# Performance work log

Measured on AMD Instinct MI355X. Metric: run time of the kernel, lower is better.

The kernel has to match this reference:

```python
import jax, jax.numpy as jnp
import numpy as np

B, L, D, H, S = 2, 2048, 1024, 16, 4
Dh = D // H
EPS = 1e-5


def setup_inputs() -> dict:
    key = jax.random.key(0)
    ks = jax.random.split(key, 12)
    sc = 0.02
    w = lambda k, shape: (jax.random.normal(k, shape, jnp.float32) * sc)
    M = 2 * S  # number of MHA blocks / dense linears
    inp = {
        "response": jax.random.normal(ks[0], (B, L, D), jnp.float32),
        "mask": jnp.broadcast_to(jnp.tril(jnp.ones((L, L), bool)), (B, L, L)),
        "Wq": w(ks[1], (M, D, D)), "bq": w(ks[2], (M, D)),
        "Wk": w(ks[3], (M, D, D)), "bk": w(ks[4], (M, D)),
        "Wv": w(ks[5], (M, D, D)), "bv": w(ks[6], (M, D)),
        "Wo": w(ks[7], (M, D, D)), "bo": w(ks[8], (M, D)),
        "Wd": w(ks[9], (M, D, D)), "bd": w(ks[10], (M, D)),
    }
    return inp


def _ln(x):
    # fresh LayerNorm(d) with default weight=1, bias=0, eps=1e-5
    m = jnp.mean(x, axis=-1, keepdims=True)
    v = jnp.mean((x - m) ** 2, axis=-1, keepdims=True)
    return (x - m) * jax.lax.rsqrt(v + EPS)


def _linear(x, W, b):
    # torch Linear: x @ W.T + b
    return jnp.einsum('bld,od->blo', x, W) + b


def _mha(x, i, mask, Wq, bq, Wk, bk, Wv, bv, Wo, bo):
    # self-attention: q = k = v = x
    split = lambda y: y.reshape(B, L, H, Dh).transpose(0, 2, 1, 3)  # (B,H,L,Dh)
    q = split(_linear(x, Wq[i], bq[i]))
    k = split(_linear(x, Wk[i], bk[i]))
    v = split(_linear(x, Wv[i], bv[i]))
    scores = jnp.einsum('bhqd,bhkd->bhqk', q, k) / jnp.sqrt(jnp.float32(Dh))
    if mask is not None:
        scores = jnp.where(mask[:, None, :, :], scores, -jnp.inf)
    p = jnp.nan_to_num(jax.nn.softmax(scores, axis=-1))
    o = jnp.einsum('bhqk,bhkd->bhqd', p, v).transpose(0, 2, 1, 3).reshape(B, L, D)
    return _linear(o, Wo[i], bo[i])


def reference(response, mask, Wq, bq, Wk, bk, Wv, bv, Wo, bo, Wd, bd):
    x = response
    for i in range(S):
        # masked self-attention + residual + LN
        x = _ln(x + _mha(x, 2 * i, mask, Wq, bq, Wk, bk, Wv, bv, Wo, bo))
        # encoder-attention sublayer (encMem is None -> unmasked self-attention)
        x = _ln(x + _mha(x, 2 * i + 1, None, Wq, bq, Wk, bk, Wv, bv, Wo, bo))
        # dense: linear[2i](LeakyReLU(linear[2i+1](x)))
        h = jax.nn.leaky_relu(_linear(x, Wd[2 * i + 1], bd[2 * i + 1]), negative_slope=0.01)
        h = _linear(h, Wd[2 * i], bd[2 * i])
        x = _ln(x + h)
    return x
```

## Files before the change

kernel.cpp:

```cpp
#include <hip/hip_runtime.h>
#include <stdint.h>
#include <stddef.h>

typedef __attribute__((ext_vector_type(8))) _Float16 f16x8;
typedef __attribute__((ext_vector_type(4))) _Float16 f16x4;
typedef __attribute__((ext_vector_type(4))) float    f32x4;

#define NB 2
#define NL 2048
#define ND 1024
#define NH 16
#define NROWS (NB*NL)

__device__ __forceinline__ void async16(void* lds, const void* g) {
  __builtin_amdgcn_global_load_lds(
      (const __attribute__((address_space(1))) void*)g,
      (__attribute__((address_space(3))) void*)lds, 16, 0, 0);
}

struct CvtArgs { const float* in[5]; _Float16* out[5]; };

__global__ __launch_bounds__(256) void cvt_all(CvtArgs a, int n16)
{
  const float* in  = a.in[blockIdx.z];
  _Float16*   out  = a.out[blockIdx.z];
  for (int i = blockIdx.x * blockDim.x + threadIdx.x; i < n16;
       i += gridDim.x * blockDim.x) {
    const f32x4* src = (const f32x4*)in + 4 * (size_t)i;
    f32x4 v0 = __builtin_nontemporal_load(src);
    f32x4 v1 = __builtin_nontemporal_load(src + 1);
    f32x4 v2 = __builtin_nontemporal_load(src + 2);
    f32x4 v3 = __builtin_nontemporal_load(src + 3);
    f16x8 o0 = {(_Float16)v0[0], (_Float16)v0[1], (_Float16)v0[2], (_Float16)v0[3],
                (_Float16)v1[0], (_Float16)v1[1], (_Float16)v1[2], (_Float16)v1[3]};
    f16x8 o1 = {(_Float16)v2[0], (_Float16)v2[1], (_Float16)v2[2], (_Float16)v2[3],
                (_Float16)v3[0], (_Float16)v3[1], (_Float16)v3[2], (_Float16)v3[3]};
    ((f16x8*)out)[2 * (size_t)i]     = o0;
    ((f16x8*)out)[2 * (size_t)i + 1] = o1;
  }
}

__global__ __launch_bounds__(256) void init_x(
    const float* __restrict__ r, _Float16* __restrict__ xh, int n8)
{
  for (int i = blockIdx.x * blockDim.x + threadIdx.x; i < n8;
       i += gridDim.x * blockDim.x) {
    float4 v0 = ((const float4*)r)[2 * i];
    float4 v1 = ((const float4*)r)[2 * i + 1];
    f16x8 o = {(_Float16)v0.x, (_Float16)v0.y, (_Float16)v0.z, (_Float16)v0.w,
               (_Float16)v1.x, (_Float16)v1.y, (_Float16)v1.z, (_Float16)v1.w};
    ((f16x8*)xh)[i] = o;
  }
}

struct GArgs {
  const _Float16* A;
  const _Float16* B[3];
  const float*    bias[3];
  void*           out[3];
  int             mode[3];
  int             ksplit;
};

__global__ __launch_bounds__(256, 2) void gemm_bt(GArgs ga)
{
  __shared__ _Float16 As[2][128 * 64];
  __shared__ _Float16 Bs[2][128 * 64];
  const int tid = threadIdx.x;
  const int w = tid >> 6, l = tid & 63;
  const int ql = l & 15, g = l >> 4;
  const int z = blockIdx.z;
  const int widx = ga.ksplit ? 0 : (blockIdx.x >> 3);
  const _Float16* Bw  = ga.B[widx];
  const float*   bias = ga.bias[widx];
  void*          outp = ga.ksplit ? ga.out[z] : ga.out[widx];
  const int      mode = ga.mode[widx];
  const int kbeg = ga.ksplit ? z * (ND / 2) : 0;
  const int kend = ga.ksplit ? kbeg + ND / 2 : ND;
  const bool dobias = (!ga.ksplit) || (z == 0);
  const int brow = blockIdx.y * 128;
  const int bcol = (blockIdx.x & 7) * 128;
  const int wm = w >> 1, wn = w & 1;
  f32x4 acc[4][4] = {};

  const int srow = w * 32 + (l >> 3);
  const int scol = ((l & 7) ^ (l >> 3)) << 3;
  const _Float16* Ag = ga.A + (size_t)(brow + srow) * ND + scol;
  const _Float16* Bg = Bw   + (size_t)(bcol + srow) * ND + scol;

#define STAGE(buf, k0_)                                                  \
  {                                                                      \
    _Float16* AsW = &As[buf][w * 2048];                                  \
    _Float16* BsW = &Bs[buf][w * 2048];                                  \
    _Pragma("unroll")                                                    \
    for (int i = 0; i < 4; ++i) {                                        \
      async16(AsW + i * 512, Ag + (size_t)i * 8 * ND + (k0_));           \
      async16(BsW + i * 512, Bg + (size_t)i * 8 * ND + (k0_));           \
    }                                                                    \
  }

  STAGE(0, kbeg);
  for (int k0 = kbeg; k0 < kend; k0 += 64) {
    const int cur = ((k0 - kbeg) >> 6) & 1;
    if (k0 + 64 < kend) {
      STAGE(cur ^ 1, k0 + 64);
      asm volatile("s_waitcnt vmcnt(8)" ::: "memory");
    } else {
      asm volatile("s_waitcnt vmcnt(0)" ::: "memory");
    }
    __builtin_amdgcn_s_barrier();
    __builtin_amdgcn_s_setprio(1);
#pragma unroll
    for (int ks = 0; ks < 64; ks += 32) {
      const int cx = (ks + g * 8) ^ ((ql & 7) << 3);
      f16x8 af[4], bf[4];
#pragma unroll
      for (int mi = 0; mi < 4; ++mi)
        af[mi] = *(const f16x8*)&As[cur][(wm * 64 + mi * 16 + ql) * 64 + cx];
#pragma unroll
      for (int nj = 0; nj < 4; ++nj)
        bf[nj] = *(const f16x8*)&Bs[cur][(wn * 64 + nj * 16 + ql) * 64 + cx];
#pragma unroll
      for (int mi = 0; mi < 4; ++mi)
#pragma unroll
        for (int nj = 0; nj < 4; ++nj)
          acc[mi][nj] = __builtin_amdgcn_mfma_f32_16x16x32_f16(
              af[mi], bf[nj], acc[mi][nj], 0, 0, 0);
    }
    __builtin_amdgcn_s_setprio(0);
    asm volatile("s_waitcnt lgkmcnt(0)" ::: "memory");
    __builtin_amdgcn_s_barrier();
  }
#undef STAGE

  const int colb = bcol + wn * 64;
  const int rowb = brow + wm * 64 + g * 4;
  if (mode == 3) {
    _Float16* vt = (_Float16*)outp;
    const int bb = rowb >> 11;
#pragma unroll
    for (int nj = 0; nj < 4; ++nj) {
      const int col = colb + nj * 16 + ql;
      const float bv = bias[col];
      const int hh = col >> 6, d = col & 63;
      _Float16* vrow = vt + ((size_t)((bb * NH + hh) * 64 + d)) * NL;
#pragma unroll
      for (int mi = 0; mi < 4; ++mi) {
        const int krow = (rowb + mi * 16) & (NL - 1);
        f16x4 o;
#pragma unroll
        for (int r = 0; r < 4; ++r) o[r] = (_Float16)(acc[mi][nj][r] + bv);
        *(f16x4*)(vrow + krow) = o;
      }
    }
  } else {
    _Float16* oh = (_Float16*)outp;
#pragma unroll
    for (int nj = 0; nj < 4; ++nj) {
      const int col = colb + nj * 16 + ql;
      const float bv = dobias ? bias[col] : 0.f;
#pragma unroll
      for (int mi = 0; mi < 4; ++mi) {
#pragma unroll
        for (int r = 0; r < 4; ++r) {
          float v = acc[mi][nj][r] + bv;
          if (mode == 2) v = v > 0.f ? v : 0.01f * v;
          oh[(size_t)(rowb + mi * 16 + r) * ND + col] = (_Float16)v;
        }
      }
    }
  }
}

template<bool CAUSAL>
__global__ __launch_bounds__(512, 4) void attn_fwd(
    const _Float16* __restrict__ Q, const _Float16* __restrict__ K,
    const _Float16* __restrict__ Vt, _Float16* __restrict__ O)
{
  __shared__ _Float16 kv[3][2][64 * 64];
  __shared__ unsigned int pls[8][8 * 34];
  const int tid = threadIdx.x;
  const int w = tid >> 6, l = tid & 63;
  const int ql = l & 15, g = l >> 4;
  const int bi = blockIdx.x;
  const int within = bi >> 3;
  const int p = (bi & 7) + 8 * (within >> 4);
  const int h = p & 15, b = p >> 4;
  const int qt_raw = within & 15;
  const int qt = (CAUSAL && b) ? (NL / 128 - 1 - qt_raw) : qt_raw;
  const int qrow = qt * 128 + w * 16 + ql;

  const _Float16* Qp = Q + (size_t)(b * NL + qrow) * ND + h * 64 + g * 8;
  const f16x8 bq0 = *(const f16x8*)Qp;
  const f16x8 bq1 = *(const f16x8*)(Qp + 32);

  const int srow = w * 8 + (l >> 3);
  const int scol = ((l & 7) ^ (l >> 3)) << 3;
  const _Float16* Kg = K  + ((size_t)(b * NL) + srow) * ND + h * 64 + scol;
  const _Float16* Vg = Vt + ((size_t)((b * NH + h) * 64 + srow)) * NL + scol;

  const int msk  = (ql & 7) << 3;
  const int offA = ql * 64 + ((     g * 8) ^ msk);
  const int offB = ql * 64 + ((32 + g * 8) ^ msk);

  unsigned int* pw = &pls[w][0];
  f32x4 ot[4] = {};
  f32x4 sum_acc = {};
  const f16x8 ones = {(_Float16)1.f, (_Float16)1.f, (_Float16)1.f, (_Float16)1.f,
                      (_Float16)1.f, (_Float16)1.f, (_Float16)1.f, (_Float16)1.f};
  const int ntiles = CAUSAL ? (qt * 2 + 2) : (NL / 64);
  const float SCL = 0.125f * 1.44269504089f;
  const float M2  = 4.0f * 1.44269504089f;

  async16(&kv[0][0][w * 512], Kg);
  async16(&kv[0][1][w * 512], Vg);

  int cbuf = 0, sbuf = 1;
  for (int kt = 0; kt < ntiles; ++kt) {
    const size_t nk0 = (size_t)((kt + 1 < ntiles) ? kt + 1 : kt) * 64;
    async16(&kv[sbuf][0][w * 512], Kg + nk0 * ND);
    async16(&kv[sbuf][1][w * 512], Vg + nk0);
    asm volatile("s_waitcnt vmcnt(2)" ::: "memory");
    __builtin_amdgcn_s_barrier();

    const _Float16* kb = &kv[cbuf][0][0];
    const _Float16* vb = &kv[cbuf][1][0];
    const int k0 = kt * 64;
    f32x4 st[4] = {};
    __builtin_amdgcn_s_setprio(1);
#pragma unroll
    for (int sub = 0; sub < 4; ++sub) {
      const f16x8 a0 = *(const f16x8*)&kb[sub * 1024 + offA];
      const f16x8 a1 = *(const f16x8*)&kb[sub * 1024 + offB];
      st[sub] = __builtin_amdgcn_mfma_f32_16x16x32_f16(a0, bq0, st[sub], 0, 0, 0);
      st[sub] = __builtin_amdgcn_mfma_f32_16x16x32_f16(a1, bq1, st[sub], 0, 0, 0);
    }
    __builtin_amdgcn_s_setprio(0);
    float pv[16];
#pragma unroll
    for (int sub = 0; sub < 4; ++sub)
#pragma unroll
      for (int r = 0; r < 4; ++r) {
        float p2 = exp2f(__builtin_fmaf(st[sub][r], SCL, -M2));
        if (CAUSAL && (k0 + sub * 16 + g * 4 + r) > qrow) p2 = 0.f;
        pv[sub * 4 + r] = p2;
      }

#pragma unroll
    for (int sub = 0; sub < 2; ++sub) {
      uint2 uu;
      uu.x = __builtin_bit_cast(unsigned int,
                __builtin_amdgcn_cvt_pkrtz(pv[sub * 4 + 0], pv[sub * 4 + 1]));
      uu.y = __builtin_bit_cast(unsigned int,
                __builtin_amdgcn_cvt_pkrtz(pv[sub * 4 + 2], pv[sub * 4 + 3]));
      *(uint2*)&pw[(sub * 4 + g) * 34 + 2 * ql] = uu;
    }
    {
      uint2 lo = *(const uint2*)&pw[(2 * g    ) * 34 + 2 * ql];
      uint2 hi = *(const uint2*)&pw[(2 * g + 1) * 34 + 2 * ql];
      uint4 ui; ui.x = lo.x; ui.y = lo.y; ui.z = hi.x; ui.w = hi.y;
      const f16x8 pf = __builtin_bit_cast(f16x8, ui);
      __builtin_amdgcn_s_setprio(1);
#pragma unroll
      for (int dt = 0; dt < 4; ++dt) {
        const f16x8 vf = *(const f16x8*)&vb[dt * 1024 + offA];
        ot[dt] = __builtin_amdgcn_mfma_f32_16x16x32_f16(vf, pf, ot[dt], 0, 0, 0);
      }
      sum_acc = __builtin_amdgcn_mfma_f32_16x16x32_f16(ones, pf, sum_acc, 0, 0, 0);
      __builtin_amdgcn_s_setprio(0);
    }
#pragma unroll
    for (int sub = 2; sub < 4; ++sub) {
      uint2 uu;
      uu.x = __builtin_bit_cast(unsigned int,
                __builtin_amdgcn_cvt_pkrtz(pv[sub * 4 + 0], pv[sub * 4 + 1]));
      uu.y = __builtin_bit_cast(unsigned int,
                __builtin_amdgcn_cvt_pkrtz(pv[sub * 4 + 2], pv[sub * 4 + 3]));
      *(uint2*)&pw[((sub - 2) * 4 + g) * 34 + 2 * ql] = uu;
    }
    {
      uint2 lo = *(const uint2*)&pw[(2 * g    ) * 34 + 2 * ql];
      uint2 hi = *(const uint2*)&pw[(2 * g + 1) * 34 + 2 * ql];
      uint4 ui; ui.x = lo.x; ui.y = lo.y; ui.z = hi.x; ui.w = hi.y;
      const f16x8 pf = __builtin_bit_cast(f16x8, ui);
      __builtin_amdgcn_s_setprio(1);
#pragma unroll
      for (int dt = 0; dt < 4; ++dt) {
        const f16x8 vf = *(const f16x8*)&vb[dt * 1024 + offB];
        ot[dt] = __builtin_amdgcn_mfma_f32_16x16x32_f16(vf, pf, ot[dt], 0, 0, 0);
      }
      sum_acc = __builtin_amdgcn_mfma_f32_16x16x32_f16(ones, pf, sum_acc, 0, 0, 0);
      __builtin_amdgcn_s_setprio(0);
    }
    cbuf = sbuf;
    sbuf = sbuf + 1 == 3 ? 0 : sbuf + 1;
  }

  const float inv = 1.f / sum_acc[0];
#pragma unroll
  for (int dt = 0; dt < 4; ++dt) {
    f16x4 o;
#pragma unroll
    for (int r = 0; r < 4; ++r) o[r] = (_Float16)(ot[dt][r] * inv);
    *(f16x4*)(O + (size_t)(b * NL + qrow) * ND + h * 64 + dt * 16 + g * 4) = o;
  }
}

template<bool FINAL>
__global__ __launch_bounds__(256) void resid_ln(
    const _Float16* __restrict__ xh_in, const _Float16* __restrict__ d0,
    const _Float16* __restrict__ d1,
    _Float16* __restrict__ xh_out, float* __restrict__ xf)
{
  const int row = blockIdx.x, tid = threadIdx.x;
  const f16x4 xv = ((const f16x4*)(xh_in + (size_t)row * ND))[tid];
  const f16x4 v0 = ((const f16x4*)(d0 + (size_t)row * ND))[tid];
  const f16x4 v1 = ((const f16x4*)(d1 + (size_t)row * ND))[tid];
  const float a = (float)xv[0] + (float)v0[0] + (float)v1[0];
  const float b = (float)xv[1] + (float)v0[1] + (float)v1[1];
  const float c = (float)xv[2] + (float)v0[2] + (float)v1[2];
  const float d = (float)xv[3] + (float)v0[3] + (float)v1[3];
  float s = a + b + c + d;
  float ss = a * a + b * b + c * c + d * d;
#pragma unroll
  for (int m = 1; m < 64; m <<= 1) {
    s  += __shfl_xor(s, m);
    ss += __shfl_xor(ss, m);
  }
  __shared__ float red[8];
  if ((tid & 63) == 0) { red[tid >> 6] = s; red[4 + (tid >> 6)] = ss; }
  __syncthreads();
  const float S  = red[0] + red[1] + red[2] + red[3];
  const float SS = red[4] + red[5] + red[6] + red[7];
  const float mean = S * (1.0f / ND);
  const float var  = SS * (1.0f / ND) - mean * mean;
  const float rstd = rsqrtf(fmaxf(var, 0.f) + 1e-5f);
  const float ya = (a - mean) * rstd, yb = (b - mean) * rstd;
  const float yc = (c - mean) * rstd, yd = (d - mean) * rstd;
  if (FINAL) {
    float4 y; y.x = ya; y.y = yb; y.z = yc; y.w = yd;
    ((float4*)(xf + (size_t)row * ND))[tid] = y;
  } else {
    f16x4 yh = {(_Float16)ya, (_Float16)yb, (_Float16)yc, (_Float16)yd};
    ((f16x4*)(xh_out + (size_t)row * ND))[tid] = yh;
  }
}

extern "C" void kernel_launch(void* const* d_in, const int* in_sizes, int n_in,
                              void* d_out, int out_size, void* d_ws, size_t ws_size,
                              hipStream_t stream)
{
  (void)in_sizes; (void)n_in; (void)out_size; (void)ws_size;
  const float* response = (const float*)d_in[0];
  const float* Wq = (const float*)d_in[2];
  const float* bq = (const float*)d_in[3];
  const float* Wk = (const float*)d_in[4];
  const float* bk = (const float*)d_in[5];
  const float* Wv = (const float*)d_in[6];
  const float* bv = (const float*)d_in[7];
  const float* Wo = (const float*)d_in[8];
  const float* bo = (const float*)d_in[9];
  const float* Wd = (const float*)d_in[10];
  const float* bd = (const float*)d_in[11];
  float* xf = (float*)d_out;

  const size_t MB = 1024 * 1024;
  char* p = (char*)d_ws;
  _Float16* Wq_h = (_Float16*)(p + 0 * MB);
  _Float16* Wk_h = (_Float16*)(p + 16 * MB);
  _Float16* Wv_h = (_Float16*)(p + 32 * MB);
  _Float16* Wo_h = (_Float16*)(p + 48 * MB);
  _Float16* Wd_h = (_Float16*)(p + 64 * MB);
  _Float16* xh   = (_Float16*)(p + 80 * MB);
  _Float16* Qh   = (_Float16*)(p + 88 * MB);
  _Float16* Kh   = (_Float16*)(p + 96 * MB);
  _Float16* Vth  = (_Float16*)(p + 104 * MB);
  _Float16* Oh   = (_Float16*)(p + 112 * MB);
  _Float16* h1   = Qh;
  _Float16* t0   = (_Float16*)(p + 96 * MB);
  _Float16* t1   = (_Float16*)(p + 104 * MB);

  const int wn16 = 8 * 1024 * 1024 / 16;
  CvtArgs ca = { { Wq, Wk, Wv, Wo, Wd }, { Wq_h, Wk_h, Wv_h, Wo_h, Wd_h } };
  cvt_all<<<dim3(1024, 1, 5), 256, 0, stream>>>(ca, wn16);
  init_x<<<1024, 256, 0, stream>>>(response, xh, NROWS * ND / 8);

  const dim3 g3(24, NROWS / 128, 1);
  const dim3 gs(8, NROWS / 128, 2);
  const dim3 gf(8, NROWS / 128, 1);
  const dim3 agrid(NL / 128 * NH * NB);

  for (int i = 0; i < 4; ++i) {
    for (int sub = 0; sub < 2; ++sub) {
      const int m = 2 * i + sub;
      const size_t wo = (size_t)m * MB;
      const size_t bf = (size_t)m * 1024;
      GArgs qkv = { xh,
                    { Wq_h + wo, Wk_h + wo, Wv_h + wo },
                    { bq + bf, bk + bf, bv + bf },
                    { Qh, Kh, Vth }, { 0, 0, 3 }, 0 };
      gemm_bt<<<g3, 256, 0, stream>>>(qkv);
      if (sub == 0) attn_fwd<true ><<<agrid, 512, 0, stream>>>(Qh, Kh, Vth, Oh);
      else          attn_fwd<false><<<agrid, 512, 0, stream>>>(Qh, Kh, Vth, Oh);
      GArgs oprj = { Oh,
                     { Wo_h + wo, nullptr, nullptr },
                     { bo + bf, nullptr, nullptr },
                     { t0, t1, nullptr }, { 0, 0, 0 }, 1 };
      gemm_bt<<<gs, 256, 0, stream>>>(oprj);
      resid_ln<false><<<NROWS, 256, 0, stream>>>(xh, t0, t1, xh, nullptr);
    }
    const size_t w1 = (size_t)(2 * i + 1) * MB, b1 = (size_t)(2 * i + 1) * 1024;
    const size_t w0 = (size_t)(2 * i) * MB,     b0 = (size_t)(2 * i) * 1024;
    GArgs f1 = { xh,
                 { Wd_h + w1, nullptr, nullptr },
                 { bd + b1, nullptr, nullptr },
                 { h1, nullptr, nullptr }, { 2, 0, 0 }, 0 };
    gemm_bt<<<gf, 256, 0, stream>>>(f1);
    GArgs f2 = { h1,
                 { Wd_h + w0, nullptr, nullptr },
                 { bd + b0, nullptr, nullptr },
                 { t0, t1, nullptr }, { 0, 0, 0 }, 1 };
    gemm_bt<<<gs, 256, 0, stream>>>(f2);
    if (i == 3) resid_ln<true ><<<NROWS, 256, 0, stream>>>(xh, t0, t1, nullptr, xf);
    else        resid_ln<false><<<NROWS, 256, 0, stream>>>(xh, t0, t1, xh, nullptr);
  }
}
```

Measured before the change: 1.184 ms.

## Single-buffer GEMM LDS tiles to raise occupancy to four blocks per CU

Replaces the double-buffered async global-to-LDS pipeline in the GEMM with a single-buffered load, wait, compute loop. LDS use is halved and launch bounds go from 2 to 4 blocks per CU. The aim is to hide memory latency through more resident blocks rather than intra-block prefetch. The trade is that each block now stalls on a full vmcnt(0) wait every K step, with no load/compute overlap inside the block.

```diff
diff --git a/kernel.cpp b/kernel.cpp
--- a/kernel.cpp
+++ b/kernel.cpp
@@ -62,10 +62,10 @@
   int             ksplit;
 };
 
-__global__ __launch_bounds__(256, 2) void gemm_bt(GArgs ga)
-{
-  __shared__ _Float16 As[2][128 * 64];
-  __shared__ _Float16 Bs[2][128 * 64];
+__global__ __launch_bounds__(256, 4) void gemm_bt(GArgs ga)
+{
+  __shared__ _Float16 As[128 * 64];
+  __shared__ _Float16 Bs[128 * 64];
   const int tid = threadIdx.x;
   const int w = tid >> 6, l = tid & 63;
   const int ql = l & 15, g = l >> 4;
@@ -88,26 +88,17 @@
   const _Float16* Ag = ga.A + (size_t)(brow + srow) * ND + scol;
   const _Float16* Bg = Bw   + (size_t)(bcol + srow) * ND + scol;
 
-#define STAGE(buf, k0_)                                                  \
-  {                                                                      \
-    _Float16* AsW = &As[buf][w * 2048];                                  \
-    _Float16* BsW = &Bs[buf][w * 2048];                                  \
-    _Pragma("unroll")                                                    \
-    for (int i = 0; i < 4; ++i) {                                        \
-      async16(AsW + i * 512, Ag + (size_t)i * 8 * ND + (k0_));           \
-      async16(BsW + i * 512, Bg + (size_t)i * 8 * ND + (k0_));           \
-    }                                                                    \
-  }
-
-  STAGE(0, kbeg);
   for (int k0 = kbeg; k0 < kend; k0 += 64) {
-    const int cur = ((k0 - kbeg) >> 6) & 1;
-    if (k0 + 64 < kend) {
-      STAGE(cur ^ 1, k0 + 64);
-      asm volatile("s_waitcnt vmcnt(8)" ::: "memory");
-    } else {
-      asm volatile("s_waitcnt vmcnt(0)" ::: "memory");
-    }
+    {
+      _Float16* AsW = &As[w * 2048];
+      _Float16* BsW = &Bs[w * 2048];
+#pragma unroll
+      for (int i = 0; i < 4; ++i) {
+        async16(AsW + i * 512, Ag + (size_t)i * 8 * ND + k0);
+        async16(BsW + i * 512, Bg + (size_t)i * 8 * ND + k0);
+      }
+    }
+    asm volatile("s_waitcnt vmcnt(0)" ::: "memory");
     __builtin_amdgcn_s_barrier();
     __builtin_amdgcn_s_setprio(1);
 #pragma unroll
@@ -116,10 +107,10 @@
       f16x8 af[4], bf[4];
 #pragma unroll
       for (int mi = 0; mi < 4; ++mi)
-        af[mi] = *(const f16x8*)&As[cur][(wm * 64 + mi * 16 + ql) * 64 + cx];
+        af[mi] = *(const f16x8*)&As[(wm * 64 + mi * 16 + ql) * 64 + cx];
 #pragma unroll
       for (int nj = 0; nj < 4; ++nj)
-        bf[nj] = *(const f16x8*)&Bs[cur][(wn * 64 + nj * 16 + ql) * 64 + cx];
+        bf[nj] = *(const f16x8*)&Bs[(wn * 64 + nj * 16 + ql) * 64 + cx];
 #pragma unroll
       for (int mi = 0; mi < 4; ++mi)
 #pragma unroll
@@ -131,7 +122,6 @@
     asm volatile("s_waitcnt lgkmcnt(0)" ::: "memory");
     __builtin_amdgcn_s_barrier();
   }
-#undef STAGE
 
   const int colb = bcol + wn * 64;
   const int rowb = brow + wm * 64 + g * 4;
```

Result: no change. 1.170 ms (-1.2%).
